# Performance work log

Measured on AMD Instinct MI355X. Metric: run time of the kernel, lower is better.

## Reference

```python
import jax, jax.numpy as jnp
import numpy as np

NUM_HEADS = 32
NUM_KV_HEADS = 8
HEAD_DIM = 128
ROPE_THETA = 1000000.0
SCALING = HEAD_DIM ** -0.5


def apply_rope_neox(x, positions):
    # x: [T, H, D], positions: [T] int
    half = HEAD_DIM // 2
    inv_freq = 1.0 / (ROPE_THETA ** (jnp.arange(0, half, dtype=jnp.float32) / half))
    freqs = positions.astype(jnp.float32)[:, None] * inv_freq[None, :]  # [T, D/2]
    cos = jnp.cos(freqs)[:, None, :]  # [T, 1, D/2]
    sin = jnp.sin(freqs)[:, None, :]
    x1, x2 = x[..., :half], x[..., half:]
    return jnp.concatenate([x1 * cos - x2 * sin, x2 * cos + x1 * sin], axis=-1)


def setup_inputs() -> dict:
    key = jax.random.key(0)
    k1, k2, k3 = jax.random.split(key, 3)
    T, H = 2048, 4096
    positions = jnp.arange(T, dtype=jnp.int32)
    hidden_states = jax.random.normal(k1, (T, H), dtype=jnp.float32)
    Wqkv = jax.random.normal(k2, (H, 6144), dtype=jnp.float32) * 0.02
    Wo = jax.random.normal(k3, (H, H), dtype=jnp.float32) * 0.02
    return {"positions": positions, "hidden_states": hidden_states, "Wqkv": Wqkv, "Wo": Wo}


def reference(positions, hidden_states, Wqkv, Wo):
    T = hidden_states.shape[0]
    q_size = NUM_HEADS * HEAD_DIM
    kv_size = NUM_KV_HEADS * HEAD_DIM
    qkv = hidden_states @ Wqkv  # [T, 6144]
    q = qkv[:, :q_size].reshape(T, NUM_HEADS, HEAD_DIM)
    k = qkv[:, q_size:q_size + kv_size].reshape(T, NUM_KV_HEADS, HEAD_DIM)
    v = qkv[:, q_size + kv_size:].reshape(T, NUM_KV_HEADS, HEAD_DIM)
    q = apply_rope_neox(q, positions)
    k = apply_rope_neox(k, positions)
    # GQA: repeat kv heads to match query heads
    rep = NUM_HEADS // NUM_KV_HEADS
    k = jnp.repeat(k, rep, axis=1)  # [T, H, D]
    v = jnp.repeat(v, rep, axis=1)
    scores = jnp.einsum('thd,shd->hts', q, k) * SCALING  # [H, T, T]
    causal = jnp.tril(jnp.ones((T, T), dtype=bool))
    scores = jnp.where(causal[None], scores, jnp.finfo(scores.dtype).min)
    attn = jax.nn.softmax(scores, axis=-1)
    out = jnp.einsum('hts,shd->thd', attn, v).reshape(T, NUM_HEADS * HEAD_DIM)
    return out @ Wo
```

## Files before the change

kernel.cpp:

```cpp
#include <hip/hip_runtime.h>
#include <math.h>

#define T_TOK 2048
#define HDIM  4096
#define QKVN  6144
#define NHEADS 32
#define HD    128
#define KV_OFF 4096
#define V_OFF  5120
#define SCALE 0.08838834764831843f

typedef __attribute__((ext_vector_type(8))) short short8;
typedef __attribute__((ext_vector_type(4))) float f32x4;
typedef __attribute__((ext_vector_type(16))) float f32x16;

__device__ __forceinline__ ushort f2bf(float f) {
    union { float f; unsigned u; } v; v.f = f;
    unsigned r = v.u + 0x7FFFu + ((v.u >> 16) & 1u);
    return (ushort)(r >> 16);
}

template <int N_, int LDK, int KC, int MODE>
__global__ __launch_bounds__(512, 2) void gemm_bf16_8ph(const ushort* __restrict__ A,
                                                        const ushort* __restrict__ B,
                                                        float* __restrict__ C0,
                                                        float* __restrict__ C1,
                                                        const int* __restrict__ pos,
                                                        ushort* __restrict__ qkB,
                                                        ushort* __restrict__ Vt) {
    __shared__ __attribute__((aligned(16))) ushort As[2][2][8192];
    __shared__ __attribute__((aligned(16))) ushort Bs[2][2][8192];

    constexpr int NT = KC / 64;
    constexpr int NBN = N_ / 256;

    const int kz = blockIdx.y;

    const int nwgx = (int)gridDim.x;
    const int bid = (int)blockIdx.x;
    const int swz = (nwgx & 7) ? bid : ((bid & 7) * (nwgx >> 3) + (bid >> 3));
    const int bm = (swz / NBN) * 256;
    const int bn = (swz % NBN) * 256;

    const int tid = (int)threadIdx.x;
    const int w = tid >> 6;
    const int l = tid & 63;
    const int hfa = w >> 2;
    const int hfb = (w & 3) >> 1;
    const int wbr64 = (w & 1) * 4096;

    const int arc = (l & 15) * 64;
    const int ac0 = ((((l >> 4) << 4)) ^ ((l & 7) << 4)) >> 1;
    const int ac1 = (((1 << 6) | ((l >> 4) << 4)) ^ ((l & 7) << 4)) >> 1;

    const int grow = w * 8 + (l >> 3);
    const int gcol = ((l & 7) ^ (l >> 3)) * 8;
    const ushort* Ag = A + (size_t)kz * KC + (size_t)(bm + grow) * LDK + gcol;
    const ushort* Bg = B + (size_t)kz * KC + (size_t)(bn + grow) * LDK + gcol;

    auto ldsA = (__attribute__((address_space(3))) char*)&As[0][0][0];
    auto ldsB = (__attribute__((address_space(3))) char*)&Bs[0][0][0];
    const int wsl = w * 1024;

#define STG2(ldsbase, gsrc, bufi, hfi, kt)                                                              \
    do {                                                                                                \
        __builtin_amdgcn_global_load_lds(                                                               \
            (const __attribute__((address_space(1))) void*)((gsrc) + (size_t)((hfi) * 128) * LDK + (kt) * 64),       \
            (__attribute__((address_space(3))) void*)((ldsbase) + (bufi) * 32768 + (hfi) * 16384 + wsl), 16, 0, 0);  \
        __builtin_amdgcn_global_load_lds(                                                               \
            (const __attribute__((address_space(1))) void*)((gsrc) + (size_t)((hfi) * 128 + 64) * LDK + (kt) * 64),  \
            (__attribute__((address_space(3))) void*)((ldsbase) + (bufi) * 32768 + (hfi) * 16384 + 8192 + wsl), 16, 0, 0); \
    } while (0)

    STG2(ldsB, Bg, 0, 0, 0);
    STG2(ldsB, Bg, 0, 1, 0);
    STG2(ldsA, Ag, 0, 0, 0);
    STG2(ldsA, Ag, 0, 1, 0);
    STG2(ldsB, Bg, 1, 0, 1);
    STG2(ldsB, Bg, 1, 1, 1);
    STG2(ldsA, Ag, 1, 0, 1);
    asm volatile("s_waitcnt vmcnt(6)" ::: "memory");
    __builtin_amdgcn_s_barrier();

    f32x4 acc[8][4];
#pragma unroll
    for (int i = 0; i < 8; i++)
#pragma unroll
        for (int j = 0; j < 4; j++) acc[i][j] = (f32x4){0.f, 0.f, 0.f, 0.f};

    short8 a0[4][2], a1[4][2], bq[4][2];

    int buf = 0;
    for (int t = 0; t < NT; ++t) {
        const int nb = buf ^ 1;
        const ushort* Abuf = &As[buf][hfa][0];
        const ushort* Bbuf = &Bs[buf][hfb][0] + wbr64;

#pragma unroll
        for (int fi = 0; fi < 4; fi++) {
            a0[fi][0] = *(const short8*)(Abuf + fi * 1024 + arc + ac0);
            a0[fi][1] = *(const short8*)(Abuf + fi * 1024 + arc + ac1);
        }
#pragma unroll
        for (int fj = 0; fj < 4; fj++) {
            bq[fj][0] = *(const short8*)(Bbuf + fj * 1024 + arc + ac0);
            bq[fj][1] = *(const short8*)(Bbuf + fj * 1024 + arc + ac1);
        }
        if (t + 1 < NT) STG2(ldsA, Ag, nb, 1, t + 1);
        __builtin_amdgcn_s_barrier();
        __builtin_amdgcn_s_setprio(1);
#pragma unroll
        for (int fi = 0; fi < 4; fi++)
#pragma unroll
            for (int fj = 0; fj < 2; fj++)
#pragma unroll
                for (int s = 0; s < 2; s++)
                    acc[fi][fj] = __builtin_amdgcn_mfma_f32_16x16x32_bf16(a0[fi][s], bq[fj][s], acc[fi][fj], 0, 0, 0);
        __builtin_amdgcn_s_setprio(0);
        __builtin_amdgcn_s_barrier();

        if (t + 2 < NT) STG2(ldsB, Bg, buf, 0, t + 2);
        __builtin_amdgcn_s_barrier();
        __builtin_amdgcn_s_setprio(1);
#pragma unroll
        for (int fi = 0; fi < 4; fi++)
#pragma unroll
            for (int fj = 2; fj < 4; fj++)
#pragma unroll
                for (int s = 0; s < 2; s++)
                    acc[fi][fj] = __builtin_amdgcn_mfma_f32_16x16x32_bf16(a0[fi][s], bq[fj][s], acc[fi][fj], 0, 0, 0);
        __builtin_amdgcn_s_setprio(0);
        __builtin_amdgcn_s_barrier();

#pragma unroll
        for (int fi = 0; fi < 4; fi++) {
            a1[fi][0] = *(const short8*)(Abuf + (fi + 4) * 1024 + arc + ac0);
            a1[fi][1] = *(const short8*)(Abuf + (fi + 4) * 1024 + arc + ac1);
        }
        if (t + 2 < NT) STG2(ldsB, Bg, buf, 1, t + 2);
        __builtin_amdgcn_s_barrier();
        __builtin_amdgcn_s_setprio(1);
#pragma unroll
        for (int fi = 0; fi < 4; fi++)
#pragma unroll
            for (int fj = 2; fj < 4; fj++)
#pragma unroll
                for (int s = 0; s < 2; s++)
                    acc[fi + 4][fj] = __builtin_amdgcn_mfma_f32_16x16x32_bf16(a1[fi][s], bq[fj][s], acc[fi + 4][fj], 0, 0, 0);
        __builtin_amdgcn_s_setprio(0);
        __builtin_amdgcn_s_barrier();

        if (t + 2 < NT) {
            STG2(ldsA, Ag, buf, 0, t + 2);
            asm volatile("s_waitcnt vmcnt(6)" ::: "memory");
        } else {
            asm volatile("s_waitcnt vmcnt(0)" ::: "memory");
        }
        __builtin_amdgcn_s_barrier();
        __builtin_amdgcn_s_setprio(1);
#pragma unroll
        for (int fi = 0; fi < 4; fi++)
#pragma unroll
            for (int fj = 0; fj < 2; fj++)
#pragma unroll
                for (int s = 0; s < 2; s++)
                    acc[fi + 4][fj] = __builtin_amdgcn_mfma_f32_16x16x32_bf16(a1[fi][s], bq[fj][s], acc[fi + 4][fj], 0, 0, 0);
        __builtin_amdgcn_s_setprio(0);
        __builtin_amdgcn_s_barrier();

        buf = nb;
    }
#undef STG2

    if constexpr (MODE == 0) {
        float* __restrict__ C = kz ? C1 : C0;
        const int cn = bn + (w & 3) * 64 + (l & 15);
        const int rm = bm + hfa * 128 + ((l >> 4) << 2);
#pragma unroll
        for (int fi = 0; fi < 8; fi++)
#pragma unroll
            for (int fj = 0; fj < 4; fj++)
#pragma unroll
                for (int r = 0; r < 4; r++)
                    C[(size_t)(rm + 16 * fi + r) * N_ + cn + 16 * fj] = acc[fi][fj][r];
    } else {
        float* Ls = (float*)&As[0][0][0];
        const bool isV = (bn >= V_OFF);
        const int q = w & 3;
        const int r4 = (l >> 4) << 2;
#pragma unroll
        for (int fi = 0; fi < 8; fi++) {
#pragma unroll
            for (int fj = 0; fj < 4; fj++)
#pragma unroll
                for (int r = 0; r < 4; r++)
                    Ls[(hfa * 16 + r4 + r) * 260 + q * 64 + (l & 15) + 16 * fj] = acc[fi][fj][r];
            __builtin_amdgcn_s_barrier();
            if (!isV) {
                const int trow = bm + hfa * 128 + 16 * fi + r4;
#pragma unroll
                for (int r = 0; r < 4; r++) {
                    const int t = trow + r;
                    const float p = (float)pos[t];
#pragma unroll
                    for (int fj = 0; fj < 4; fj++) {
                        const int cr = q * 64 + (l & 15) + 16 * fj;
                        const int dd = cr & 127;
                        const int d64 = dd & 63;
                        const float own = acc[fi][fj][r];
                        const float prt = Ls[(hfa * 16 + r4 + r) * 260 + (cr ^ 64)];
                        const float invf = exp2f(-(float)d64 * (19.931568569324174f / 64.0f));
                        const float ang = p * invf;
                        const float cf = __cosf(ang), sf = __sinf(ang);
                        const float o = (dd < 64) ? (own * cf - prt * sf) : (own * cf + prt * sf);
                        const float sc = (bn + cr < KV_OFF) ? SCALE : 1.0f;
                        qkB[(size_t)t * QKVN + bn + cr] = f2bf(o * sc);
                    }
                }
            } else {
                const int vcr = tid >> 1;
                const int hh = tid & 1;
                union { ushort u[16]; short8 s[2]; } tmp;
#pragma unroll
                for (int rr = 0; rr < 16; rr++)
                    tmp.u[rr] = f2bf(Ls[(hh * 16 + rr) * 260 + vcr]);
                ushort* dst = Vt + (size_t)(bn - V_OFF + vcr) * 2048 + bm + hh * 128 + 16 * fi;
                *(short8*)dst = tmp.s[0];
                *(short8*)(dst + 8) = tmp.s[1];
            }
            __builtin_amdgcn_s_barrier();
        }
    }
}

__global__ __launch_bounds__(256) void add_f32(float* __restrict__ out,
                                               const float* __restrict__ p) {
    const int i = (blockIdx.x * 256 + threadIdx.x) * 4;
    float4 a = *(const float4*)(out + i);
    float4 b = *(const float4*)(p + i);
    a.x += b.x; a.y += b.y; a.z += b.z; a.w += b.w;
    *(float4*)(out + i) = a;
}

__global__ __launch_bounds__(256) void cast_bf16(const float* __restrict__ in,
                                                 ushort* __restrict__ outp) {
    const int i = (blockIdx.x * 256 + threadIdx.x) * 4;
    float4 v = *(const float4*)(in + i);
    ushort4 o = {f2bf(v.x), f2bf(v.y), f2bf(v.z), f2bf(v.w)};
    *(ushort4*)(outp + i) = o;
}

template <int K_, int N_>
__global__ __launch_bounds__(256) void transpose_cast(const float* __restrict__ W,
                                                      ushort* __restrict__ WT) {
    __shared__ float T[32 * 65];
    const int k0 = blockIdx.y * 32;
    const int n0 = blockIdx.x * 64;
    const int x = threadIdx.x & 63;
    const int y = threadIdx.x >> 6;
#pragma unroll
    for (int p = 0; p < 8; p++) {
        const int kk = p * 4 + y;
        T[kk * 65 + x] = W[(size_t)(k0 + kk) * N_ + n0 + x];
    }
    __syncthreads();
#pragma unroll
    for (int q = 0; q < 4; q++) {
        const int nl = q * 16 + (threadIdx.x >> 4);
        const int k2 = (threadIdx.x & 15) * 2;
        ushort2 o = {f2bf(T[k2 * 65 + nl]), f2bf(T[(k2 + 1) * 65 + nl])};
        *(ushort2*)&WT[(size_t)(n0 + nl) * K_ + k0 + k2] = o;
    }
}

__global__ __launch_bounds__(256, 2) void flash_attn_mfma(
        const ushort* __restrict__ qkB,
        const ushort* __restrict__ Vt,
        ushort* __restrict__ attnB) {
    __shared__ ushort Kf[2][16 * 512];
    __shared__ ushort Vf[2][16 * 512];

    const int b = blockIdx.x;
    const int half = b >> 8;
    const int rest = b & 255;
    const int h = rest >> 3;
    const int q8 = rest & 7;
    const int qi = half ? (15 - q8) : q8;
    const int kvh = h >> 2;

    const int tid = threadIdx.x;
    const int w = tid >> 6;
    const int l = tid & 63;
    const int l31 = l & 31;
    const int hf = l >> 5;

    const int qg = qi * 128 + w * 32 + l31;

    short8 qf[8];
    {
        const ushort* qrow = qkB + (size_t)qg * QKVN + h * HD + hf * 8;
#pragma unroll
        for (int kt = 0; kt < 8; kt++)
            qf[kt] = *(const short8*)(qrow + kt * 16);
    }

    f32x16 O[4];
#pragma unroll
    for (int dt = 0; dt < 4; dt++)
#pragma unroll
        for (int r = 0; r < 16; r++) O[dt][r] = 0.f;
    float mcur = -INFINITY, lcur = 0.f;

    const ushort* kbase = qkB + (size_t)l31 * QKVN + KV_OFF + kvh * HD + (2 * w) * 16 + hf * 8;
    const ushort* vbase = Vt + ((size_t)(kvh * 128 + w * 32 + l31)) * 2048 + hf * 8;

    auto ldsK = (__attribute__((address_space(3))) char*)&Kf[0][0];
    auto ldsV = (__attribute__((address_space(3))) char*)&Vf[0][0];

    const int nst = 2 * qi + 2;
    const int mylast = (4 * qi + w) >> 1;

#define GLD(src, dst) __builtin_amdgcn_global_load_lds(                              \
        (const __attribute__((address_space(1))) void*)(src),                        \
        (__attribute__((address_space(3))) void*)(dst), 16, 0, 0)

#define AST64(j, bb)                                                                 \
    do {                                                                             \
        const ushort* kg0 = kbase + (size_t)(j) * 64 * QKVN;                         \
        const ushort* kg1 = kg0 + (size_t)32 * QKVN;                                 \
        GLD(kg0,      ldsK + (bb) * 16384 + (2 * w) * 1024);                         \
        GLD(kg0 + 16, ldsK + (bb) * 16384 + (2 * w + 1) * 1024);                     \
        GLD(kg1,      ldsK + (bb) * 16384 + (8 + 2 * w) * 1024);                     \
        GLD(kg1 + 16, ldsK + (bb) * 16384 + (8 + 2 * w + 1) * 1024);                 \
        const ushort* vg = vbase + (j) * 64;                                         \
        GLD(vg,       ldsV + (bb) * 16384 + (4 * w + 0) * 1024);                     \
        GLD(vg + 16,  ldsV + (bb) * 16384 + (4 * w + 1) * 1024);                     \
        GLD(vg + 32,  ldsV + (bb) * 16384 + (4 * w + 2) * 1024);                     \
        GLD(vg + 48,  ldsV + (bb) * 16384 + (4 * w + 3) * 1024);                     \
    } while (0)

    AST64(0, 0);

    for (int j = 0; j < nst; j++) {
        const int buf = j & 1;
        __builtin_amdgcn_s_barrier();
        if (j + 1 < nst) {
            AST64(j + 1, buf ^ 1);
            asm volatile("s_waitcnt vmcnt(8)" ::: "memory");
        } else {
            asm volatile("s_waitcnt vmcnt(0)" ::: "memory");
        }
        __builtin_amdgcn_s_barrier();

        if (j <= mylast) {
            const ushort* Kb = &Kf[buf][0];
            const ushort* Vb = &Vf[buf][0];
            f32x16 S0, S1;
#pragma unroll
            for (int r = 0; r < 16; r++) { S0[r] = 0.f; S1[r] = 0.f; }
            __builtin_amdgcn_s_setprio(1);
#pragma unroll
            for (int kt = 0; kt < 8; kt++) {
                short8 k0 = *(const short8*)(Kb + kt * 512 + l * 8);
                S0 = __builtin_amdgcn_mfma_f32_32x32x16_bf16(k0, qf[kt], S0, 0, 0, 0);
            }
#pragma unroll
            for (int kt = 0; kt < 8; kt++) {
                short8 k1 = *(const short8*)(Kb + (8 + kt) * 512 + l * 8);
                S1 = __builtin_amdgcn_mfma_f32_32x32x16_bf16(k1, qf[kt], S1, 0, 0, 0);
            }
            __builtin_amdgcn_s_setprio(0);

            if (j == mylast) {
                const int sb = j * 64 + 4 * hf;
#pragma unroll
                for (int r = 0; r < 16; r++) {
                    const int sg = sb + (r & 3) + 8 * (r >> 2);
                    if (sg > qg) S0[r] = -INFINITY;
                    if (sg + 32 > qg) S1[r] = -INFINITY;
                }
            }
            float rmax = S0[0];
#pragma unroll
            for (int r = 1; r < 16; r++) rmax = fmaxf(rmax, S0[r]);
#pragma unroll
            for (int r = 0; r < 16; r++) rmax = fmaxf(rmax, S1[r]);
            rmax = fmaxf(rmax, __shfl_xor(rmax, 32));

            const unsigned long long need = __ballot(rmax > mcur + 8.0f);
            float mnew, alpha;
            if (need == 0) { mnew = mcur; alpha = 1.0f; }
            else { mnew = fmaxf(mcur, rmax); alpha = __expf(mcur - mnew); }

            float rsum = 0.f;
#pragma unroll
            for (int r = 0; r < 16; r++) {
                S0[r] = __expf(S0[r] - mnew);
                rsum += S0[r];
            }
#pragma unroll
            for (int r = 0; r < 16; r++) {
                S1[r] = __expf(S1[r] - mnew);
                rsum += S1[r];
            }
            rsum += __shfl_xor(rsum, 32);
            lcur = lcur * alpha + rsum;
            mcur = mnew;

            if (need != 0) {
#pragma unroll
                for (int dt = 0; dt < 4; dt++)
#pragma unroll
                    for (int r = 0; r < 16; r++) O[dt][r] *= alpha;
            }

            short8 Pf[4];
            {
                unsigned pk[8], rk[8];
#pragma unroll
                for (int g = 0; g < 4; g++) {
                    pk[2 * g]     = (unsigned)f2bf(S0[4 * g])     | ((unsigned)f2bf(S0[4 * g + 1]) << 16);
                    pk[2 * g + 1] = (unsigned)f2bf(S0[4 * g + 2]) | ((unsigned)f2bf(S0[4 * g + 3]) << 16);
                }
#pragma unroll
                for (int i = 0; i < 8; i++) rk[i] = (unsigned)__shfl_xor((int)pk[i], 32);
#pragma unroll
                for (int kt2 = 0; kt2 < 2; kt2++) {
                    const int g = 2 * kt2 + hf;
                    union { unsigned u[4]; short8 s; } cvt;
                    cvt.u[0] = hf ? rk[2 * g]     : pk[2 * g];
                    cvt.u[1] = hf ? rk[2 * g + 1] : pk[2 * g + 1];
                    cvt.u[2] = hf ? pk[2 * g]     : rk[2 * g];
                    cvt.u[3] = hf ? pk[2 * g + 1] : rk[2 * g + 1];
                    Pf[kt2] = cvt.s;
                }
#pragma unroll
                for (int g = 0; g < 4; g++) {
                    pk[2 * g]     = (unsigned)f2bf(S1[4 * g])     | ((unsigned)f2bf(S1[4 * g + 1]) << 16);
                    pk[2 * g + 1] = (unsigned)f2bf(S1[4 * g + 2]) | ((unsigned)f2bf(S1[4 * g + 3]) << 16);
                }
#pragma unroll
                for (int i = 0; i < 8; i++) rk[i] = (unsigned)__shfl_xor((int)pk[i], 32);
#pragma unroll
                for (int kt2 = 0; kt2 < 2; kt2++) {
                    const int g = 2 * kt2 + hf;
                    union { unsigned u[4]; short8 s; } cvt;
                    cvt.u[0] = hf ? rk[2 * g]     : pk[2 * g];
                    cvt.u[1] = hf ? rk[2 * g + 1] : pk[2 * g + 1];
                    cvt.u[2] = hf ? pk[2 * g]     : rk[2 * g];
                    cvt.u[3] = hf ? pk[2 * g + 1] : rk[2 * g + 1];
                    Pf[2 + kt2] = cvt.s;
                }
            }

            __builtin_amdgcn_s_setprio(1);
#pragma unroll
            for (int dt = 0; dt < 4; dt++)
#pragma unroll
                for (int ks = 0; ks < 4; ks++) {
                    short8 afV = *(const short8*)(Vb + (dt * 4 + ks) * 512 + l * 8);
                    O[dt] = __builtin_amdgcn_mfma_f32_32x32x16_bf16(afV, Pf[ks], O[dt], 0, 0, 0);
                }
            __builtin_amdgcn_s_setprio(0);
        }
    }
#undef AST64
#undef GLD

    const float inv = 1.0f / lcur;
    ushort* orow = attnB + (size_t)qg * HDIM + h * HD + 4 * hf;
#pragma unroll
    for (int dt = 0; dt < 4; dt++)
#pragma unroll
        for (int rg = 0; rg < 4; rg++) {
            ushort4 o;
            o.x = f2bf(O[dt][4 * rg + 0] * inv);
            o.y = f2bf(O[dt][4 * rg + 1] * inv);
            o.z = f2bf(O[dt][4 * rg + 2] * inv);
            o.w = f2bf(O[dt][4 * rg + 3] * inv);
            *(ushort4*)(orow + dt * 32 + 8 * rg) = o;
        }
}

__global__ __launch_bounds__(256) void rope_kernel(const int* __restrict__ pos,
                                                   float* __restrict__ qkv) {
    const int t = blockIdx.x;
    const int head = blockIdx.y * 4 + (threadIdx.x >> 6);
    const int d = threadIdx.x & 63;
    const float p = (float)pos[t];
    const float invf = exp2f(-(float)d * (19.931568569324174f / 64.0f));
    const float f = p * invf;
    const float c = cosf(f), s = sinf(f);
    float* base = qkv + (size_t)t * QKVN + head * HD;
    const float x1 = base[d];
    const float x2 = base[d + 64];
    base[d]      = x1 * c - x2 * s;
    base[d + 64] = x2 * c + x1 * s;
}

#define DOT4(acc, a, b) acc += (a).x*(b).x + (a).y*(b).y + (a).z*(b).z + (a).w*(b).w
#define FMA4(o, p, v) { (o).x += (p)*(v).x; (o).y += (p)*(v).y; (o).z += (p)*(v).z; (o).w += (p)*(v).w; }

__global__ __launch_bounds__(256, 2) void flash_attn_f32(const float* __restrict__ qkv,
                                                         float* __restrict__ out) {
    __shared__ float Qs[64 * 132];
    __shared__ float KVs[32 * 132];
    __shared__ float Ps[64 * 34];
    const int b = blockIdx.x;
    const int half = (b >> 9) & 1;
    const int rest = b & 511;
    const int h = rest >> 4;
    const int qlo = rest & 15;
    const int qi = half ? (31 - qlo) : qlo;
    const int kvh = h >> 2;
    const int tid = threadIdx.x;
    const int tx = tid & 7;
    const int ty = tid >> 3;
    {
        const float* qbase = qkv + (size_t)(qi * 64) * QKVN + h * HD;
#pragma unroll
        for (int r = 0; r < 8; r++) {
            int idx = r * 256 + tid;
            int qrow = idx >> 5;
            int d = (idx & 31) * 4;
            float4 v = *(const float4*)(qbase + (size_t)qrow * QKVN + d);
            v.x *= SCALE; v.y *= SCALE; v.z *= SCALE; v.w *= SCALE;
            *(float4*)(Qs + qrow * 132 + d) = v;
        }
    }
    float m[2], lsm[2];
    float4 O[2][4];
#pragma unroll
    for (int i = 0; i < 2; i++) {
        m[i] = -INFINITY; lsm[i] = 0.f;
#pragma unroll
        for (int jj = 0; jj < 4; jj++) O[i][jj] = make_float4(0.f, 0.f, 0.f, 0.f);
    }
    const float* kbase = qkv + KV_OFF + kvh * HD;
    const float* vbase = qkv + V_OFF + kvh * HD;
    const int qg0 = qi * 64 + ty;
    const int nst = 2 * qi + 2;
    for (int st = 0; st < nst; st++) {
        __syncthreads();
#pragma unroll
        for (int r = 0; r < 4; r++) {
            int idx = r * 256 + tid;
            int srow = idx >> 5;
            int d = (idx & 31) * 4;
            *(float4*)(KVs + srow * 132 + d) =
                *(const float4*)(kbase + (size_t)(st * 32 + srow) * QKVN + d);
        }
        __syncthreads();
        float S[2][4];
#pragma unroll
        for (int i = 0; i < 2; i++)
#pragma unroll
            for (int j = 0; j < 4; j++) S[i][j] = 0.f;
#pragma unroll 4
        for (int kk = 0; kk < HD; kk += 4) {
            float4 q0 = *(const float4*)(Qs + ty * 132 + kk);
            float4 q1 = *(const float4*)(Qs + (ty + 32) * 132 + kk);
            float4 k0 = *(const float4*)(KVs + tx * 132 + kk);
            float4 k1 = *(const float4*)(KVs + (tx + 8) * 132 + kk);
            float4 k2 = *(const float4*)(KVs + (tx + 16) * 132 + kk);
            float4 k3 = *(const float4*)(KVs + (tx + 24) * 132 + kk);
            DOT4(S[0][0], q0, k0); DOT4(S[0][1], q0, k1);
            DOT4(S[0][2], q0, k2); DOT4(S[0][3], q0, k3);
            DOT4(S[1][0], q1, k0); DOT4(S[1][1], q1, k1);
            DOT4(S[1][2], q1, k2); DOT4(S[1][3], q1, k3);
        }
        const int sg0 = st * 32 + tx;
        float alpha[2];
#pragma unroll
        for (int i = 0; i < 2; i++) {
            const int qg = qg0 + 32 * i;
            float rmax = -INFINITY;
#pragma unroll
            for (int j = 0; j < 4; j++) {
                if (sg0 + 8 * j > qg) S[i][j] = -INFINITY;
                rmax = fmaxf(rmax, S[i][j]);
            }
#pragma unroll
            for (int off = 1; off < 8; off <<= 1)
                rmax = fmaxf(rmax, __shfl_xor(rmax, off));
            const float mnew = fmaxf(m[i], rmax);
            alpha[i] = __expf(m[i] - mnew);
            float rsum = 0.f;
#pragma unroll
            for (int j = 0; j < 4; j++) {
                S[i][j] = __expf(S[i][j] - mnew);
                rsum += S[i][j];
            }
#pragma unroll
            for (int off = 1; off < 8; off <<= 1)
                rsum += __shfl_xor(rsum, off);
            lsm[i] = lsm[i] * alpha[i] + rsum;
            m[i] = mnew;
        }
#pragma unroll
        for (int i = 0; i < 2; i++)
#pragma unroll
            for (int j = 0; j < 4; j++)
                Ps[(ty + 32 * i) * 34 + tx + 8 * j] = S[i][j];
        __syncthreads();
#pragma unroll
        for (int r = 0; r < 4; r++) {
            int idx = r * 256 + tid;
            int srow = idx >> 5;
            int d = (idx & 31) * 4;
            *(float4*)(KVs + srow * 132 + d) =
                *(const float4*)(vbase + (size_t)(st * 32 + srow) * QKVN + d);
        }
        __syncthreads();
#pragma unroll
        for (int i = 0; i < 2; i++) {
            const float a = alpha[i];
#pragma unroll
            for (int jj = 0; jj < 4; jj++) {
                O[i][jj].x *= a; O[i][jj].y *= a; O[i][jj].z *= a; O[i][jj].w *= a;
            }
        }
#pragma unroll 4
        for (int s = 0; s < 32; s++) {
            float p0 = Ps[ty * 34 + s];
            float p1 = Ps[(ty + 32) * 34 + s];
            const float* vr = KVs + s * 132 + 4 * tx;
            float4 v0 = *(const float4*)(vr);
            float4 v1 = *(const float4*)(vr + 32);
            float4 v2 = *(const float4*)(vr + 64);
            float4 v3 = *(const float4*)(vr + 96);
            FMA4(O[0][0], p0, v0); FMA4(O[0][1], p0, v1);
            FMA4(O[0][2], p0, v2); FMA4(O[0][3], p0, v3);
            FMA4(O[1][0], p1, v0); FMA4(O[1][1], p1, v1);
            FMA4(O[1][2], p1, v2); FMA4(O[1][3], p1, v3);
        }
    }
#pragma unroll
    for (int i = 0; i < 2; i++) {
        const float inv = 1.0f / lsm[i];
        float* orow = out + (size_t)(qi * 64 + ty + 32 * i) * HDIM + h * HD + 4 * tx;
#pragma unroll
        for (int jj = 0; jj < 4; jj++) {
            float4 wv = O[i][jj];
            wv.x *= inv; wv.y *= inv; wv.z *= inv; wv.w *= inv;
            *(float4*)(orow + 32 * jj) = wv;
        }
    }
}

template <int N_, int K_>
__global__ __launch_bounds__(256) void sgemm(const float* __restrict__ A,
                                             const float* __restrict__ B,
                                             float* __restrict__ C) {
    __shared__ float As[8][128];
    __shared__ float Bs[8][128];
    const int tid = threadIdx.x;
    const int bm = blockIdx.y * 128;
    const int bn = blockIdx.x * 128;
    const int tx = tid & 15;
    const int ty = tid >> 4;
    const int lm = tid >> 1;
    const int lkq = (tid & 1) * 4;
    const int lr = tid >> 5;
    const int lnq = (tid & 31) * 4;
    float acc[8][8];
#pragma unroll
    for (int i = 0; i < 8; i++)
#pragma unroll
        for (int j = 0; j < 8; j++) acc[i][j] = 0.f;
    const float* Aptr = A + (size_t)(bm + lm) * K_ + lkq;
    const float* Bptr = B + (size_t)lr * N_ + bn + lnq;
    for (int k0 = 0; k0 < K_; k0 += 8) {
        float4 av = *(const float4*)Aptr;
        float4 bv = *(const float4*)Bptr;
        __syncthreads();
        As[lkq + 0][lm] = av.x;
        As[lkq + 1][lm] = av.y;
        As[lkq + 2][lm] = av.z;
        As[lkq + 3][lm] = av.w;
        *(float4*)&Bs[lr][lnq] = bv;
        __syncthreads();
        Aptr += 8;
        Bptr += (size_t)8 * N_;
#pragma unroll
        for (int kk = 0; kk < 8; kk++) {
            float4 a0 = *(const float4*)&As[kk][ty * 4];
            float4 a1 = *(const float4*)&As[kk][64 + ty * 4];
            float4 b0 = *(const float4*)&Bs[kk][tx * 4];
            float4 b1 = *(const float4*)&Bs[kk][64 + tx * 4];
            float a[8] = {a0.x, a0.y, a0.z, a0.w, a1.x, a1.y, a1.z, a1.w};
            float bb[8] = {b0.x, b0.y, b0.z, b0.w, b1.x, b1.y, b1.z, b1.w};
#pragma unroll
            for (int i = 0; i < 8; i++)
#pragma unroll
                for (int j = 0; j < 8; j++) acc[i][j] += a[i] * bb[j];
        }
    }
#pragma unroll
    for (int i = 0; i < 8; i++) {
        int row = bm + ((i < 4) ? (ty * 4 + i) : (64 + ty * 4 + i - 4));
        float4 c0 = {acc[i][0], acc[i][1], acc[i][2], acc[i][3]};
        float4 c1 = {acc[i][4], acc[i][5], acc[i][6], acc[i][7]};
        *(float4*)&C[(size_t)row * N_ + bn + tx * 4] = c0;
        *(float4*)&C[(size_t)row * N_ + bn + 64 + tx * 4] = c1;
    }
}

extern "C" void kernel_launch(void* const* d_in, const int* in_sizes, int n_in,
                              void* d_out, int out_size, void* d_ws, size_t ws_size,
                              hipStream_t stream) {
    const int*   positions = (const int*)d_in[0];
    const float* hidden    = (const float*)d_in[1];
    const float* Wqkv      = (const float*)d_in[2];
    const float* Wo        = (const float*)d_in[3];
    float* out = (float*)d_out;

    char* ws = (char*)d_ws;
    ushort* qkB   = (ushort*)ws;
    ushort* Vt    = (ushort*)(ws + 25165824);
    ushort* attnB = (ushort*)(ws + 29360128);
    float*  Pk    = (float*)(ws + 46137344);
    ushort* WqkvT = (ushort*)(ws + 50331648);
    ushort* WoT   = (ushort*)(ws + 100663296);
    ushort* hA    = (ushort*)(ws + 134217728);
    const size_t NEEDED = 163577856;

    if (ws_size >= NEEDED) {
        cast_bf16<<<dim3((T_TOK * HDIM) / 1024), 256, 0, stream>>>(hidden, hA);
        transpose_cast<HDIM, QKVN><<<dim3(QKVN / 64, HDIM / 32), 256, 0, stream>>>(Wqkv, WqkvT);
        transpose_cast<HDIM, HDIM><<<dim3(HDIM / 64, HDIM / 32), 256, 0, stream>>>(Wo, WoT);
        gemm_bf16_8ph<QKVN, HDIM, HDIM, 1>
            <<<dim3((T_TOK / 256) * (QKVN / 256), 1), 512, 0, stream>>>(
                hA, WqkvT, nullptr, nullptr, positions, qkB, Vt);
        flash_attn_mfma<<<dim3(512), 256, 0, stream>>>(qkB, Vt, attnB);
        gemm_bf16_8ph<HDIM, HDIM, HDIM / 2, 0>
            <<<dim3((T_TOK / 256) * (HDIM / 256), 2), 512, 0, stream>>>(
                attnB, WoT, out, Pk, nullptr, nullptr, nullptr);
        add_f32<<<dim3((T_TOK * HDIM) / 1024), 256, 0, stream>>>(out, Pk);
    } else {
        float* qkv  = (float*)ws;
        float* attn = qkv + (size_t)T_TOK * QKVN;
        sgemm<QKVN, HDIM><<<dim3(QKVN / 128, T_TOK / 128), 256, 0, stream>>>(hidden, Wqkv, qkv);
        rope_kernel<<<dim3(T_TOK, 10), 256, 0, stream>>>(positions, qkv);
        flash_attn_f32<<<dim3(1024), 256, 0, stream>>>(qkv, attn);
        sgemm<HDIM, HDIM><<<dim3(HDIM / 128, T_TOK / 128), 256, 0, stream>>>(attn, Wo, out);
    }
}
```

Before: 604.2 us.

## Replace split-K output GEMM with 256x128-tile kernel and widen transpose tiles

The output projection used a 256x256-tile GEMM split across K in two halves, with a partial buffer and a separate add kernel. It is replaced by a new 256x128-tile GEMM with a triple-buffered global-to-LDS pipeline. That kernel launches 256 workgroups over the full K, so the fp32 partial write and the extra add pass go away. The weight transpose-cast kernel now handles 64x64 tiles and writes 16-element vector stores, cutting launch count and store instructions. Each workgroup now does a longer K loop with smaller tiles, which lowers arithmetic intensity per tile.

```diff
diff --git a/kernel.cpp b/kernel.cpp
--- a/kernel.cpp
+++ b/kernel.cpp
@@ -233,13 +233,144 @@
     }
 }
 
-__global__ __launch_bounds__(256) void add_f32(float* __restrict__ out,
-                                               const float* __restrict__ p) {
-    const int i = (blockIdx.x * 256 + threadIdx.x) * 4;
-    float4 a = *(const float4*)(out + i);
-    float4 b = *(const float4*)(p + i);
-    a.x += b.x; a.y += b.y; a.z += b.z; a.w += b.w;
-    *(float4*)(out + i) = a;
+template <int N_, int LDK, int KC>
+__global__ __launch_bounds__(512, 2) void gemm_bf16_n128(const ushort* __restrict__ A,
+                                                         const ushort* __restrict__ B,
+                                                         float* __restrict__ C) {
+    __shared__ __attribute__((aligned(16))) ushort As[3][2][8192];
+    __shared__ __attribute__((aligned(16))) ushort Bs[3][8192];
+
+    constexpr int NT = KC / 64;
+    constexpr int NBN = N_ / 128;
+
+    const int nwgx = (int)gridDim.x;
+    const int bid = (int)blockIdx.x;
+    const int swz = (nwgx & 7) ? bid : ((bid & 7) * (nwgx >> 3) + (bid >> 3));
+    const int bm = (swz / NBN) * 256;
+    const int bn = (swz % NBN) * 128;
+
+    const int tid = (int)threadIdx.x;
+    const int w = tid >> 6;
+    const int l = tid & 63;
+    const int hfa = w >> 2;
+    const int wq = w & 3;
+
+    const int arc = (l & 15) * 64;
+    const int ac0 = ((((l >> 4) << 4)) ^ ((l & 7) << 4)) >> 1;
+    const int ac1 = (((1 << 6) | ((l >> 4) << 4)) ^ ((l & 7) << 4)) >> 1;
+
+    const int grow = w * 8 + (l >> 3);
+    const int gcol = ((l & 7) ^ (l >> 3)) * 8;
+    const ushort* Ag = A + (size_t)(bm + grow) * LDK + gcol;
+    const ushort* Bg = B + (size_t)(bn + grow) * LDK + gcol;
+
+    auto ldsA = (__attribute__((address_space(3))) char*)&As[0][0][0];
+    auto ldsBs = (__attribute__((address_space(3))) char*)&Bs[0][0];
+    const int wsl = w * 1024;
+
+#define GLD16(src, dst) __builtin_amdgcn_global_load_lds(                            \
+        (const __attribute__((address_space(1))) void*)(src),                        \
+        (__attribute__((address_space(3))) void*)(dst), 16, 0, 0)
+
+#define STGA2(bufi, hfi, kt)                                                          \
+    do {                                                                              \
+        GLD16(Ag + (size_t)((hfi) * 128) * LDK + (kt) * 64,                           \
+              ldsA + (bufi) * 32768 + (hfi) * 16384 + wsl);                           \
+        GLD16(Ag + (size_t)((hfi) * 128 + 64) * LDK + (kt) * 64,                      \
+              ldsA + (bufi) * 32768 + (hfi) * 16384 + 8192 + wsl);                    \
+    } while (0)
+
+#define STGB2(bufi, kt)                                                               \
+    do {                                                                              \
+        GLD16(Bg + (kt) * 64,                ldsBs + (bufi) * 16384 + wsl);           \
+        GLD16(Bg + (size_t)64 * LDK + (kt) * 64, ldsBs + (bufi) * 16384 + 8192 + wsl);\
+    } while (0)
+
+    STGB2(0, 0);
+    STGA2(0, 0, 0);
+    STGA2(0, 1, 0);
+    STGA2(1, 1, 1);
+    STGB2(1, 1);
+    STGA2(1, 0, 1);
+    asm volatile("s_waitcnt vmcnt(6)" ::: "memory");
+    __builtin_amdgcn_s_barrier();
+
+    f32x4 acc[8][2];
+#pragma unroll
+    for (int i = 0; i < 8; i++)
+#pragma unroll
+        for (int j = 0; j < 2; j++) acc[i][j] = (f32x4){0.f, 0.f, 0.f, 0.f};
+
+    short8 a0[4][2], a1[4][2], bq[2][2];
+
+    int b0 = 0;
+    for (int t = 0; t < NT; ++t) {
+        const int b2 = (b0 >= 1) ? (b0 - 1) : 2;
+        const ushort* Abuf = &As[b0][hfa][0];
+        const ushort* Bbuf = &Bs[b0][0] + wq * 2048;
+
+#pragma unroll
+        for (int fi = 0; fi < 4; fi++) {
+            a0[fi][0] = *(const short8*)(Abuf + fi * 1024 + arc + ac0);
+            a0[fi][1] = *(const short8*)(Abuf + fi * 1024 + arc + ac1);
+        }
+#pragma unroll
+        for (int fj = 0; fj < 2; fj++) {
+            bq[fj][0] = *(const short8*)(Bbuf + fj * 1024 + arc + ac0);
+            bq[fj][1] = *(const short8*)(Bbuf + fj * 1024 + arc + ac1);
+        }
+        if (t + 2 < NT) STGA2(b2, 1, t + 2);
+        __builtin_amdgcn_s_barrier();
+        __builtin_amdgcn_s_setprio(1);
+#pragma unroll
+        for (int fi = 0; fi < 4; fi++)
+#pragma unroll
+            for (int fj = 0; fj < 2; fj++)
+#pragma unroll
+                for (int s = 0; s < 2; s++)
+                    acc[fi][fj] = __builtin_amdgcn_mfma_f32_16x16x32_bf16(a0[fi][s], bq[fj][s], acc[fi][fj], 0, 0, 0);
+        __builtin_amdgcn_s_setprio(0);
+        __builtin_amdgcn_s_barrier();
+
+#pragma unroll
+        for (int fi = 0; fi < 4; fi++) {
+            a1[fi][0] = *(const short8*)(Abuf + (fi + 4) * 1024 + arc + ac0);
+            a1[fi][1] = *(const short8*)(Abuf + (fi + 4) * 1024 + arc + ac1);
+        }
+        if (t + 2 < NT) {
+            STGB2(b2, t + 2);
+            STGA2(b2, 0, t + 2);
+            asm volatile("s_waitcnt vmcnt(6)" ::: "memory");
+        } else {
+            asm volatile("s_waitcnt vmcnt(0)" ::: "memory");
+        }
+        __builtin_amdgcn_s_barrier();
+        __builtin_amdgcn_s_setprio(1);
+#pragma unroll
+        for (int fi = 0; fi < 4; fi++)
+#pragma unroll
+            for (int fj = 0; fj < 2; fj++)
+#pragma unroll
+                for (int s = 0; s < 2; s++)
+                    acc[fi + 4][fj] = __builtin_amdgcn_mfma_f32_16x16x32_bf16(a1[fi][s], bq[fj][s], acc[fi + 4][fj], 0, 0, 0);
+        __builtin_amdgcn_s_setprio(0);
+        __builtin_amdgcn_s_barrier();
+
+        b0 = (b0 + 1 == 3) ? 0 : (b0 + 1);
+    }
+#undef STGA2
+#undef STGB2
+#undef GLD16
+
+    const int cn = bn + wq * 32 + (l & 15);
+    const int rm = bm + hfa * 128 + ((l >> 4) << 2);
+#pragma unroll
+    for (int fi = 0; fi < 8; fi++)
+#pragma unroll
+        for (int fj = 0; fj < 2; fj++)
+#pragma unroll
+            for (int r = 0; r < 4; r++)
+                C[(size_t)(rm + 16 * fi + r) * N_ + cn + 16 * fj] = acc[fi][fj][r];
 }
 
 __global__ __launch_bounds__(256) void cast_bf16(const float* __restrict__ in,
@@ -253,24 +384,25 @@
 template <int K_, int N_>
 __global__ __launch_bounds__(256) void transpose_cast(const float* __restrict__ W,
                                                       ushort* __restrict__ WT) {
-    __shared__ float T[32 * 65];
-    const int k0 = blockIdx.y * 32;
+    __shared__ float T[64][65];
+    const int k0 = blockIdx.y * 64;
     const int n0 = blockIdx.x * 64;
     const int x = threadIdx.x & 63;
     const int y = threadIdx.x >> 6;
 #pragma unroll
-    for (int p = 0; p < 8; p++) {
+    for (int p = 0; p < 16; p++) {
         const int kk = p * 4 + y;
-        T[kk * 65 + x] = W[(size_t)(k0 + kk) * N_ + n0 + x];
+        T[kk][x] = W[(size_t)(k0 + kk) * N_ + n0 + x];
     }
     __syncthreads();
-#pragma unroll
-    for (int q = 0; q < 4; q++) {
-        const int nl = q * 16 + (threadIdx.x >> 4);
-        const int k2 = (threadIdx.x & 15) * 2;
-        ushort2 o = {f2bf(T[k2 * 65 + nl]), f2bf(T[(k2 + 1) * 65 + nl])};
-        *(ushort2*)&WT[(size_t)(n0 + nl) * K_ + k0 + k2] = o;
-    }
+    const int nl = threadIdx.x >> 2;
+    const int kc = (threadIdx.x & 3) * 16;
+    union { ushort u[16]; short8 s[2]; } tmp;
+#pragma unroll
+    for (int i = 0; i < 16; i++) tmp.u[i] = f2bf(T[kc + i][nl]);
+    ushort* dst = &WT[(size_t)(n0 + nl) * K_ + k0 + kc];
+    *(short8*)dst = tmp.s[0];
+    *(short8*)(dst + 8) = tmp.s[1];
 }
 
 __global__ __launch_bounds__(256, 2) void flash_attn_mfma(
@@ -719,7 +851,6 @@
     ushort* qkB   = (ushort*)ws;
     ushort* Vt    = (ushort*)(ws + 25165824);
     ushort* attnB = (ushort*)(ws + 29360128);
-    float*  Pk    = (float*)(ws + 46137344);
     ushort* WqkvT = (ushort*)(ws + 50331648);
     ushort* WoT   = (ushort*)(ws + 100663296);
     ushort* hA    = (ushort*)(ws + 134217728);
@@ -727,16 +858,14 @@
 
     if (ws_size >= NEEDED) {
         cast_bf16<<<dim3((T_TOK * HDIM) / 1024), 256, 0, stream>>>(hidden, hA);
-        transpose_cast<HDIM, QKVN><<<dim3(QKVN / 64, HDIM / 32), 256, 0, stream>>>(Wqkv, WqkvT);
-        transpose_cast<HDIM, HDIM><<<dim3(HDIM / 64, HDIM / 32), 256, 0, stream>>>(Wo, WoT);
+        transpose_cast<HDIM, QKVN><<<dim3(QKVN / 64, HDIM / 64), 256, 0, stream>>>(Wqkv, WqkvT);
+        transpose_cast<HDIM, HDIM><<<dim3(HDIM / 64, HDIM / 64), 256, 0, stream>>>(Wo, WoT);
         gemm_bf16_8ph<QKVN, HDIM, HDIM, 1>
             <<<dim3((T_TOK / 256) * (QKVN / 256), 1), 512, 0, stream>>>(
                 hA, WqkvT, nullptr, nullptr, positions, qkB, Vt);
         flash_attn_mfma<<<dim3(512), 256, 0, stream>>>(qkB, Vt, attnB);
-        gemm_bf16_8ph<HDIM, HDIM, HDIM / 2, 0>
-            <<<dim3((T_TOK / 256) * (HDIM / 256), 2), 512, 0, stream>>>(
-                attnB, WoT, out, Pk, nullptr, nullptr, nullptr);
-        add_f32<<<dim3((T_TOK * HDIM) / 1024), 256, 0, stream>>>(out, Pk);
+        gemm_bf16_n128<HDIM, HDIM, HDIM>
+            <<<dim3((T_TOK / 256) * (HDIM / 128)), 512, 0, stream>>>(attnB, WoT, out);
     } else {
         float* qkv  = (float*)ws;
         float* attn = qkv + (size_t)T_TOK * QKVN;
```

Result: faster. 588.7 us (-2.6%).
